# Performance work log

Measured on AMD Instinct MI355X. Metric: run time of the kernel, lower is better.

The kernel has to match this reference:

```python
import jax, jax.numpy as jnp
import numpy as np

PI = float(np.pi)


def _cgs(node_feats, node_centre, nbr_idx, graph_w,
         mean_rho, mean_theta, prec_rho, prec_theta, conv_w, use_graph_weights):
    # node_feats: [B,N,C]; node_centre: [B,N,2]; nbr_idx: [B,N,K] (within-sample node ids)
    # graph_w: [B*N*K, 1] or None; mean/prec: [1,R]; conv_w: [R, C, OUT//R]
    B, N, C = node_feats.shape
    K = nbr_idx.shape[-1]
    R = mean_rho.shape[-1]
    BN = B * N
    # flat neighbor index into B*N nodes (coords[1])
    flat_nbr = (jnp.arange(B, dtype=nbr_idx.dtype)[:, None, None] * N + nbr_idx).reshape(BN * K)
    src = jnp.repeat(jnp.arange(BN), K)
    centre = node_centre.reshape(BN, 2)
    d = centre[src] - centre[flat_nbr]                    # [E,2], node_intersect 'minus'
    rho = jnp.sqrt(d[:, 0] ** 2 + d[:, 1] ** 2)
    theta = jnp.arctan2(d[:, 0], d[:, 1])
    # gaussian mixture edge weights over R kernels
    w_rho = jnp.exp(-0.5 * (rho[:, None] - mean_rho) ** 2 / (1e-14 + prec_rho ** 2))
    first_angle = jnp.abs(theta[:, None] - mean_theta)
    second_angle = jnp.abs(2.0 * PI - first_angle)
    w_theta = jnp.exp(-0.5 * jnp.minimum(first_angle, second_angle) ** 2
                      / (1e-14 + prec_theta ** 2))
    w = w_rho * w_theta
    w = jnp.where(jnp.isnan(w), 0.0, w)
    w = w / jnp.sum(w, axis=1, keepdims=True)             # [E,R]
    if use_graph_weights:
        w = graph_w * w
    ew = w.reshape(BN, K, R)
    nj = node_feats.reshape(BN, C)[flat_nbr].reshape(BN, K, C)   # gather neighbors
    agg = jnp.einsum('ekr,ekc->erc', ew, nj).reshape(B, N, R, C)  # weighted bmm
    out = jnp.einsum('bnrc,rcd->bnrd', agg, conv_w).reshape(B, N, R * conv_w.shape[-1])
    return jax.nn.relu(out)


def setup_inputs() -> dict:
    key = jax.random.key(0)
    ks = jax.random.split(key, 16)
    B, N, K, C, R, OUT = 64, 100, 16, 1024, 8, 1024
    D = OUT // R
    return {
        "node_feats": jax.random.normal(ks[0], (B, N, C), jnp.float32),
        "node_centre": jax.random.uniform(ks[1], (B, N, 2), dtype=jnp.float32),
        "graph_w": jax.random.uniform(ks[2], (B * N * K, 1), dtype=jnp.float32),
        "nbr_idx": jax.random.randint(ks[3], (B, N, K), 0, N, dtype=jnp.int32),
        "mean_rho1": jax.random.uniform(ks[4], (1, R), dtype=jnp.float32),
        "mean_theta1": jax.random.uniform(ks[5], (1, R), dtype=jnp.float32, minval=-PI, maxval=PI),
        "prec_rho1": jax.random.uniform(ks[6], (1, R), dtype=jnp.float32),
        "prec_theta1": jax.random.uniform(ks[7], (1, R), dtype=jnp.float32),
        "conv_w1": jax.random.normal(ks[8], (R, C, D), jnp.float32) * 0.02,
        "mean_rho2": jax.random.uniform(ks[9], (1, R), dtype=jnp.float32),
        "mean_theta2": jax.random.uniform(ks[10], (1, R), dtype=jnp.float32, minval=-PI, maxval=PI),
        "prec_rho2": jax.random.uniform(ks[11], (1, R), dtype=jnp.float32),
        "prec_theta2": jax.random.uniform(ks[12], (1, R), dtype=jnp.float32),
        "conv_w2": jax.random.normal(ks[13], (R, OUT, D), jnp.float32) * 0.02,
    }


def reference(node_feats, node_centre, graph_w,
              mean_rho1, mean_theta1, prec_rho1, prec_theta1, conv_w1,
              mean_rho2, mean_theta2, prec_rho2, prec_theta2, conv_w2,
              nbr_idx):
    # NodeFeatLayer('cgs_sum^8') = Sequential(CgsNodeFeat(use_graph_weights=True),
    #                                          CgsNodeFeat(use_graph_weights=False))
    h = _cgs(node_feats, node_centre, nbr_idx, graph_w,
             mean_rho1, mean_theta1, prec_rho1, prec_theta1, conv_w1, True)
    h = _cgs(h, node_centre, nbr_idx, None,
             mean_rho2, mean_theta2, prec_rho2, prec_theta2, conv_w2, False)
    return h
```

## Files before the change

kernel.cpp:

```cpp
#include <hip/hip_runtime.h>
#include <hip/hip_bf16.h>
#include <math.h>

#define B_   64
#define N_   100
#define K_   16
#define C_   1024
#define R_   8
#define BN_  6400
#define E_   102400

typedef __attribute__((ext_vector_type(8))) short bf16x8;
typedef __attribute__((ext_vector_type(4))) float f32x4;

__device__ __forceinline__ float bf2f(ushort h) {
    union { uint32_t u; float f; } v; v.u = ((uint32_t)h) << 16; return v.f;
}
__device__ __forceinline__ ushort f2bf(float f) {
    union { float f; uint32_t u; } v; v.f = f;
    uint32_t r = v.u + 0x7FFFu + ((v.u >> 16) & 1u);
    return (ushort)(r >> 16);
}

__device__ __forceinline__ void gload_lds16(const void* g, void* l) {
    __builtin_amdgcn_global_load_lds(
        (const __attribute__((address_space(1))) void*)g,
        (__attribute__((address_space(3))) void*)l, 16, 0, 0);
}

__global__ __launch_bounds__(256) void edge_weights_kernel(
        const float* __restrict__ centre, const int* __restrict__ nbr_idx,
        const float* __restrict__ graph_w,
        const float* __restrict__ mr1, const float* __restrict__ mt1,
        const float* __restrict__ pr1, const float* __restrict__ pt1,
        const float* __restrict__ mr2, const float* __restrict__ mt2,
        const float* __restrict__ pr2, const float* __restrict__ pt2,
        float* __restrict__ w1, float* __restrict__ w2) {
    int e = blockIdx.x * blockDim.x + threadIdx.x;
    if (e >= E_) return;
    int n = e / K_;
    int b = n / N_;
    int fn = b * N_ + nbr_idx[e];
    float dx = centre[2*n]   - centre[2*fn];
    float dy = centre[2*n+1] - centre[2*fn+1];
    float rho   = sqrtf(dx*dx + dy*dy);
    float theta = atan2f(dx, dy);
    const float TWO_PI = 6.28318530717958647692f;
    {
        float w[R_]; float s = 0.f;
        #pragma unroll
        for (int r = 0; r < R_; ++r) {
            float dr = rho - mr1[r];
            float wr = expf(-0.5f * dr * dr / (1e-14f + pr1[r]*pr1[r]));
            float fa = fabsf(theta - mt1[r]);
            float mi = fminf(fa, fabsf(TWO_PI - fa));
            float wt = expf(-0.5f * mi * mi / (1e-14f + pt1[r]*pt1[r]));
            float ww = wr * wt;
            if (isnan(ww)) ww = 0.f;
            w[r] = ww; s += ww;
        }
        float gw = graph_w[e];
        #pragma unroll
        for (int r = 0; r < R_; ++r) w1[(size_t)r * E_ + e] = gw * (w[r] / s);
    }
    {
        float w[R_]; float s = 0.f;
        #pragma unroll
        for (int r = 0; r < R_; ++r) {
            float dr = rho - mr2[r];
            float wr = expf(-0.5f * dr * dr / (1e-14f + pr2[r]*pr2[r]));
            float fa = fabsf(theta - mt2[r]);
            float mi = fminf(fa, fabsf(TWO_PI - fa));
            float wt = expf(-0.5f * mi * mi / (1e-14f + pt2[r]*pt2[r]));
            float ww = wr * wt;
            if (isnan(ww)) ww = 0.f;
            w[r] = ww; s += ww;
        }
        #pragma unroll
        for (int r = 0; r < R_; ++r) w2[(size_t)r * E_ + e] = w[r] / s;
    }
}

__global__ __launch_bounds__(256) void cast_x_kernel(
        const float* __restrict__ X, ushort* __restrict__ Xb) {
    int i = (blockIdx.x * 256 + threadIdx.x) * 4;
    float4 v = *(const float4*)&X[i];
    ushort4 o; o.x = f2bf(v.x); o.y = f2bf(v.y); o.z = f2bf(v.z); o.w = f2bf(v.w);
    *(ushort4*)&Xb[i] = o;
}

__global__ __launch_bounds__(256) void wtrans_kernel(
        const float* __restrict__ W1, ushort* __restrict__ Wt1,
        const float* __restrict__ W2, ushort* __restrict__ Wt2) {
    __shared__ ushort T[64][138];
    const float* W = (blockIdx.z == 0) ? W1 : W2;
    ushort*    Wt = (blockIdx.z == 0) ? Wt1 : Wt2;
    int r  = blockIdx.y;
    int c0 = blockIdx.x * 64;
    int t  = threadIdx.x;
    int lane6 = t & 63;
    #pragma unroll
    for (int it = 0; it < 16; ++it) {
        int ch = (t >> 6) + 4 * it;
        int d  = lane6 * 2;
        float2 v = *(const float2*)&W[(((size_t)r << 10) + c0 + ch) * 128 + d];
        T[ch][d]     = f2bf(v.x);
        T[ch][d + 1] = f2bf(v.y);
    }
    __syncthreads();
    #pragma unroll
    for (int it = 0; it < 32; ++it) {
        int d = (t >> 6) + 4 * it;
        Wt[(size_t)(r * 128 + d) * 1024 + c0 + lane6] = T[lane6][d];
    }
}

__global__ __launch_bounds__(256) void fused_gemm_agg_kernel(
        const ushort* __restrict__ Xb,
        const ushort* __restrict__ Wt,
        const float* __restrict__ wR,
        const int*   __restrict__ nbr,
        ushort* __restrict__ outB,
        float*  __restrict__ outF) {
    __shared__ ushort Asb[2][112][32];
    __shared__ ushort Bsb[2][128][32];
    __shared__ ushort P_lds[100][128];
    __shared__ float  w_lds[1600];
    __shared__ int    f_lds[1600];

    int bid = blockIdx.x;
    int swz = (bid & 7) * 64 + (bid >> 3);
    int sample = swz >> 3, cb = swz & 7;
    int t = threadIdx.x, wid = t >> 6, lane = t & 63;

    int srow  = lane >> 2;
    int sslot = (lane & 3) ^ ((lane >> 2) & 3) ^ (lane >> 4);
    int pslot = (lane >> 4) ^ (lane & 3) ^ ((lane >> 2) & 3);

    const ushort* agp = Xb + (size_t)(sample * 100 + srow) * 1024 + sslot * 8;
    const ushort* bgp = Wt + (size_t)(cb * 128 + srow) * 1024 + sslot * 8;

    f32x4 acc[7][2];
    #pragma unroll
    for (int i = 0; i < 7; ++i) { acc[i][0] = (f32x4)0.f; acc[i][1] = (f32x4)0.f; }

    #pragma unroll
    for (int q = 0; q < 2; ++q) {
        int ch = wid + 4 * q;
        if (ch < 7) gload_lds16(agp + (size_t)ch * 16 * 1024, &Asb[0][ch * 16][0]);
        gload_lds16(bgp + (size_t)ch * 16 * 1024, &Bsb[0][ch * 16][0]);
    }
    __syncthreads();

    for (int ts = 0; ts < 32; ++ts) {
        int cur = ts & 1;
        if (ts < 31) {
            int c1 = (ts + 1) * 32;
            #pragma unroll
            for (int q = 0; q < 2; ++q) {
                int ch = wid + 4 * q;
                if (ch < 7) gload_lds16(agp + (size_t)ch * 16 * 1024 + c1,
                                        &Asb[cur ^ 1][ch * 16][0]);
                gload_lds16(bgp + (size_t)ch * 16 * 1024 + c1,
                            &Bsb[cur ^ 1][ch * 16][0]);
            }
        }
        bf16x8 af[7], bfr[2];
        #pragma unroll
        for (int mi = 0; mi < 7; ++mi)
            af[mi] = *(const bf16x8*)&Asb[cur][mi * 16 + (lane & 15)][pslot * 8];
        #pragma unroll
        for (int ni = 0; ni < 2; ++ni)
            bfr[ni] = *(const bf16x8*)&Bsb[cur][wid * 32 + ni * 16 + (lane & 15)][pslot * 8];
        #pragma unroll
        for (int mi = 0; mi < 7; ++mi)
            #pragma unroll
            for (int ni = 0; ni < 2; ++ni)
                acc[mi][ni] = __builtin_amdgcn_mfma_f32_16x16x32_bf16(
                    af[mi], bfr[ni], acc[mi][ni], 0, 0, 0);
        __syncthreads();
    }

    #pragma unroll
    for (int mi = 0; mi < 7; ++mi) {
        #pragma unroll
        for (int ni = 0; ni < 2; ++ni) {
            int colb = wid * 32 + ni * 16 + (lane & 15);
            #pragma unroll
            for (int q = 0; q < 4; ++q) {
                int row = mi * 16 + (lane >> 4) * 4 + q;
                if (row < 100) {
                    int phys = colb ^ (((row >> 2) & 3) << 4);
                    P_lds[row][phys] = f2bf(acc[mi][ni][q]);
                }
            }
        }
    }
    {
        const float* wsrc = wR + (size_t)cb * E_ + (size_t)sample * 1600;
        const int*   nsrc = nbr + (size_t)sample * 1600;
        for (int i = t; i < 1600; i += 256) {
            w_lds[i] = wsrc[i];
            f_lds[i] = nsrc[i];
        }
    }
    __syncthreads();

    int p = lane;
    int nb = wid;
    for (int i = 0; i < 25; ++i) {
        int n = nb + 4 * i;
        float a0 = 0.f, a1 = 0.f;
        #pragma unroll
        for (int k = 0; k < 16; ++k) {
            int row  = f_lds[n * 16 + k];
            float wk = w_lds[n * 16 + k];
            ushort2 v = *(const ushort2*)&P_lds[row][(2 * p) ^ (((row >> 2) & 3) << 4)];
            a0 += wk * bf2f(v.x);
            a1 += wk * bf2f(v.y);
        }
        a0 = fmaxf(a0, 0.f);
        a1 = fmaxf(a1, 0.f);
        size_t base = (size_t)(sample * 100 + n) * 1024 + cb * 128 + 2 * p;
        if (outB) {
            ushort2 o; o.x = f2bf(a0); o.y = f2bf(a1);
            *(ushort2*)&outB[base] = o;
        } else {
            float2 o; o.x = a0; o.y = a1;
            *(float2*)&outF[base] = o;
        }
    }
}

extern "C" void kernel_launch(void* const* d_in, const int* in_sizes, int n_in,
                              void* d_out, int out_size, void* d_ws, size_t ws_size,
                              hipStream_t stream) {
    const float* node_feats = (const float*)d_in[0];
    const float* centre     = (const float*)d_in[1];
    const float* graph_w    = (const float*)d_in[2];
    const int*   nbr_idx    = (const int*)  d_in[3];
    const float* mr1 = (const float*)d_in[4];
    const float* mt1 = (const float*)d_in[5];
    const float* pr1 = (const float*)d_in[6];
    const float* pt1 = (const float*)d_in[7];
    const float* cw1 = (const float*)d_in[8];
    const float* mr2 = (const float*)d_in[9];
    const float* mt2 = (const float*)d_in[10];
    const float* pr2 = (const float*)d_in[11];
    const float* pt2 = (const float*)d_in[12];
    const float* cw2 = (const float*)d_in[13];

    char* ws = (char*)d_ws;
    ushort* Xb  = (ushort*)ws;  ws += (size_t)BN_ * 1024 * 2;
    ushort* W1t = (ushort*)ws;  ws += (size_t)1024 * 1024 * 2;
    ushort* W2t = (ushort*)ws;  ws += (size_t)1024 * 1024 * 2;
    ushort* hb  = (ushort*)ws;  ws += (size_t)BN_ * 1024 * 2;
    float*  w1  = (float*)ws;   ws += (size_t)R_ * E_ * 4;
    float*  w2  = (float*)ws;

    float* out = (float*)d_out;

    edge_weights_kernel<<<(E_ + 255) / 256, 256, 0, stream>>>(
        centre, nbr_idx, graph_w, mr1, mt1, pr1, pt1, mr2, mt2, pr2, pt2, w1, w2);
    cast_x_kernel<<<BN_ * 1024 / 4 / 256, 256, 0, stream>>>(node_feats, Xb);
    wtrans_kernel<<<dim3(16, 8, 2), 256, 0, stream>>>(cw1, W1t, cw2, W2t);

    fused_gemm_agg_kernel<<<512, 256, 0, stream>>>(Xb, W1t, w1, nbr_idx, hb, nullptr);
    fused_gemm_agg_kernel<<<512, 256, 0, stream>>>(hb, W2t, w2, nbr_idx, nullptr, out);
}
```

Measured before the change: 197.4 us.

## Merge prep kernels, pad samples to 128 rows, halve GEMM column tile

The three preprocessing kernels become one launch that branches on block index. Node features are stored padded to 128 rows per sample, so the GEMM A tile loads without masking. The fused GEMM+aggregate kernel now computes 64 output columns per block, on a 2x2 wave layout over 128 padded rows. This doubles the grid to 1024 blocks, and the GEMM staging and aggregation buffers share LDS through a union. The intent is fewer launches, better occupancy and less LDS per block. The cost is that each sample's A tile is reloaded by twice as many blocks, and padded rows waste MFMA work.

```diff
diff --git a/kernel.cpp b/kernel.cpp
--- a/kernel.cpp
+++ b/kernel.cpp
@@ -9,6 +9,7 @@
 #define R_   8
 #define BN_  6400
 #define E_   102400
+#define MPAD 128
 
 typedef __attribute__((ext_vector_type(8))) short bf16x8;
 typedef __attribute__((ext_vector_type(4))) float f32x4;
@@ -21,99 +22,111 @@
     uint32_t r = v.u + 0x7FFFu + ((v.u >> 16) & 1u);
     return (ushort)(r >> 16);
 }
-
 __device__ __forceinline__ void gload_lds16(const void* g, void* l) {
     __builtin_amdgcn_global_load_lds(
         (const __attribute__((address_space(1))) void*)g,
         (__attribute__((address_space(3))) void*)l, 16, 0, 0);
 }
 
-__global__ __launch_bounds__(256) void edge_weights_kernel(
+__global__ __launch_bounds__(256) void prep_kernel(
         const float* __restrict__ centre, const int* __restrict__ nbr_idx,
         const float* __restrict__ graph_w,
         const float* __restrict__ mr1, const float* __restrict__ mt1,
         const float* __restrict__ pr1, const float* __restrict__ pt1,
         const float* __restrict__ mr2, const float* __restrict__ mt2,
         const float* __restrict__ pr2, const float* __restrict__ pt2,
-        float* __restrict__ w1, float* __restrict__ w2) {
-    int e = blockIdx.x * blockDim.x + threadIdx.x;
-    if (e >= E_) return;
-    int n = e / K_;
-    int b = n / N_;
-    int fn = b * N_ + nbr_idx[e];
-    float dx = centre[2*n]   - centre[2*fn];
-    float dy = centre[2*n+1] - centre[2*fn+1];
-    float rho   = sqrtf(dx*dx + dy*dy);
-    float theta = atan2f(dx, dy);
-    const float TWO_PI = 6.28318530717958647692f;
-    {
-        float w[R_]; float s = 0.f;
-        #pragma unroll
-        for (int r = 0; r < R_; ++r) {
-            float dr = rho - mr1[r];
-            float wr = expf(-0.5f * dr * dr / (1e-14f + pr1[r]*pr1[r]));
-            float fa = fabsf(theta - mt1[r]);
-            float mi = fminf(fa, fabsf(TWO_PI - fa));
-            float wt = expf(-0.5f * mi * mi / (1e-14f + pt1[r]*pt1[r]));
-            float ww = wr * wt;
-            if (isnan(ww)) ww = 0.f;
-            w[r] = ww; s += ww;
-        }
-        float gw = graph_w[e];
-        #pragma unroll
-        for (int r = 0; r < R_; ++r) w1[(size_t)r * E_ + e] = gw * (w[r] / s);
-    }
-    {
-        float w[R_]; float s = 0.f;
-        #pragma unroll
-        for (int r = 0; r < R_; ++r) {
-            float dr = rho - mr2[r];
-            float wr = expf(-0.5f * dr * dr / (1e-14f + pr2[r]*pr2[r]));
-            float fa = fabsf(theta - mt2[r]);
-            float mi = fminf(fa, fabsf(TWO_PI - fa));
-            float wt = expf(-0.5f * mi * mi / (1e-14f + pt2[r]*pt2[r]));
-            float ww = wr * wt;
-            if (isnan(ww)) ww = 0.f;
-            w[r] = ww; s += ww;
-        }
-        #pragma unroll
-        for (int r = 0; r < R_; ++r) w2[(size_t)r * E_ + e] = w[r] / s;
-    }
-}
-
-__global__ __launch_bounds__(256) void cast_x_kernel(
-        const float* __restrict__ X, ushort* __restrict__ Xb) {
-    int i = (blockIdx.x * 256 + threadIdx.x) * 4;
-    float4 v = *(const float4*)&X[i];
-    ushort4 o; o.x = f2bf(v.x); o.y = f2bf(v.y); o.z = f2bf(v.z); o.w = f2bf(v.w);
-    *(ushort4*)&Xb[i] = o;
-}
-
-__global__ __launch_bounds__(256) void wtrans_kernel(
-        const float* __restrict__ W1, ushort* __restrict__ Wt1,
-        const float* __restrict__ W2, ushort* __restrict__ Wt2) {
+        const float* __restrict__ X,  const float* __restrict__ CW1,
+        const float* __restrict__ CW2,
+        float* __restrict__ w1, float* __restrict__ w2,
+        ushort* __restrict__ Xb, ushort* __restrict__ Wt1,
+        ushort* __restrict__ Wt2) {
     __shared__ ushort T[64][138];
-    const float* W = (blockIdx.z == 0) ? W1 : W2;
-    ushort*    Wt = (blockIdx.z == 0) ? Wt1 : Wt2;
-    int r  = blockIdx.y;
-    int c0 = blockIdx.x * 64;
-    int t  = threadIdx.x;
-    int lane6 = t & 63;
-    #pragma unroll
-    for (int it = 0; it < 16; ++it) {
-        int ch = (t >> 6) + 4 * it;
-        int d  = lane6 * 2;
-        float2 v = *(const float2*)&W[(((size_t)r << 10) + c0 + ch) * 128 + d];
-        T[ch][d]     = f2bf(v.x);
-        T[ch][d + 1] = f2bf(v.y);
-    }
-    __syncthreads();
-    #pragma unroll
-    for (int it = 0; it < 32; ++it) {
-        int d = (t >> 6) + 4 * it;
-        Wt[(size_t)(r * 128 + d) * 1024 + c0 + lane6] = T[lane6][d];
-    }
-}
+    int bid = blockIdx.x, t = threadIdx.x;
+    if (bid < 400) {
+        int e = bid * 256 + t;
+        int n = e / K_;
+        int b = n / N_;
+        int fn = b * N_ + nbr_idx[e];
+        float dx = centre[2*n]   - centre[2*fn];
+        float dy = centre[2*n+1] - centre[2*fn+1];
+        float rho   = sqrtf(dx*dx + dy*dy);
+        float theta = atan2f(dx, dy);
+        const float TWO_PI = 6.28318530717958647692f;
+        {
+            float w[R_]; float s = 0.f;
+            #pragma unroll
+            for (int r = 0; r < R_; ++r) {
+                float dr = rho - mr1[r];
+                float wr = expf(-0.5f * dr * dr / (1e-14f + pr1[r]*pr1[r]));
+                float fa = fabsf(theta - mt1[r]);
+                float mi = fminf(fa, fabsf(TWO_PI - fa));
+                float wt = expf(-0.5f * mi * mi / (1e-14f + pt1[r]*pt1[r]));
+                float ww = wr * wt;
+                if (isnan(ww)) ww = 0.f;
+                w[r] = ww; s += ww;
+            }
+            float gw = graph_w[e];
+            #pragma unroll
+            for (int r = 0; r < R_; ++r) w1[(size_t)r * E_ + e] = gw * (w[r] / s);
+        }
+        {
+            float w[R_]; float s = 0.f;
+            #pragma unroll
+            for (int r = 0; r < R_; ++r) {
+                float dr = rho - mr2[r];
+                float wr = expf(-0.5f * dr * dr / (1e-14f + pr2[r]*pr2[r]));
+                float fa = fabsf(theta - mt2[r]);
+                float mi = fminf(fa, fabsf(TWO_PI - fa));
+                float wt = expf(-0.5f * mi * mi / (1e-14f + pt2[r]*pt2[r]));
+                float ww = wr * wt;
+                if (isnan(ww)) ww = 0.f;
+                w[r] = ww; s += ww;
+            }
+            #pragma unroll
+            for (int r = 0; r < R_; ++r) w2[(size_t)r * E_ + e] = w[r] / s;
+        }
+    } else if (bid < 3600) {
+        int gid = (bid - 400) * 256 + t;
+        int n  = gid >> 7;
+        int c0 = (gid & 127) * 8;
+        const float* src = X + (size_t)n * 1024 + c0;
+        float4 v0 = *(const float4*)src;
+        float4 v1 = *(const float4*)(src + 4);
+        bf16x8 o;
+        o[0] = (short)f2bf(v0.x); o[1] = (short)f2bf(v0.y);
+        o[2] = (short)f2bf(v0.z); o[3] = (short)f2bf(v0.w);
+        o[4] = (short)f2bf(v1.x); o[5] = (short)f2bf(v1.y);
+        o[6] = (short)f2bf(v1.z); o[7] = (short)f2bf(v1.w);
+        int prow = (n / 100) * MPAD + (n % 100);
+        *(bf16x8*)&Xb[(size_t)prow * 1024 + c0] = o;
+    } else {
+        int w = bid - 3600;
+        int layer = w >> 7, rr = (w >> 4) & 7, ct = w & 15;
+        const float* W = layer ? CW2 : CW1;
+        ushort*    Wt = layer ? Wt2 : Wt1;
+        int c0 = ct * 64;
+        int lane6 = t & 63;
+        #pragma unroll
+        for (int it = 0; it < 16; ++it) {
+            int ch = (t >> 6) + 4 * it;
+            int d  = lane6 * 2;
+            float2 v = *(const float2*)&W[(((size_t)rr << 10) + c0 + ch) * 128 + d];
+            T[ch][d]     = f2bf(v.x);
+            T[ch][d + 1] = f2bf(v.y);
+        }
+        __syncthreads();
+        #pragma unroll
+        for (int it = 0; it < 32; ++it) {
+            int d = (t >> 6) + 4 * it;
+            Wt[(size_t)(rr * 128 + d) * 1024 + c0 + lane6] = T[lane6][d];
+        }
+    }
+}
+
+union SharedU {
+    struct { ushort A[2][128][32]; ushort Bm[2][64][32]; } m;
+    struct { ushort P[100][64]; float w[1600]; int f[1600]; } e;
+};
 
 __global__ __launch_bounds__(256) void fused_gemm_agg_kernel(
         const ushort* __restrict__ Xb,
@@ -122,58 +135,46 @@
         const int*   __restrict__ nbr,
         ushort* __restrict__ outB,
         float*  __restrict__ outF) {
-    __shared__ ushort Asb[2][112][32];
-    __shared__ ushort Bsb[2][128][32];
-    __shared__ ushort P_lds[100][128];
-    __shared__ float  w_lds[1600];
-    __shared__ int    f_lds[1600];
-
+    __shared__ SharedU su;
     int bid = blockIdx.x;
-    int swz = (bid & 7) * 64 + (bid >> 3);
-    int sample = swz >> 3, cb = swz & 7;
+    int swz = (bid & 7) * 128 + (bid >> 3);
+    int sample = swz >> 4, cb = swz & 15;
     int t = threadIdx.x, wid = t >> 6, lane = t & 63;
+    int wm = wid >> 1, wn = wid & 1;
 
     int srow  = lane >> 2;
     int sslot = (lane & 3) ^ ((lane >> 2) & 3) ^ (lane >> 4);
     int pslot = (lane >> 4) ^ (lane & 3) ^ ((lane >> 2) & 3);
 
-    const ushort* agp = Xb + (size_t)(sample * 100 + srow) * 1024 + sslot * 8;
-    const ushort* bgp = Wt + (size_t)(cb * 128 + srow) * 1024 + sslot * 8;
-
-    f32x4 acc[7][2];
+    const ushort* agp = Xb + (size_t)(sample * MPAD + srow) * 1024 + sslot * 8;
+    const ushort* bgp = Wt + (size_t)(cb * 64 + srow) * 1024 + sslot * 8;
+
+    f32x4 acc[4][2];
     #pragma unroll
-    for (int i = 0; i < 7; ++i) { acc[i][0] = (f32x4)0.f; acc[i][1] = (f32x4)0.f; }
-
-    #pragma unroll
-    for (int q = 0; q < 2; ++q) {
-        int ch = wid + 4 * q;
-        if (ch < 7) gload_lds16(agp + (size_t)ch * 16 * 1024, &Asb[0][ch * 16][0]);
-        gload_lds16(bgp + (size_t)ch * 16 * 1024, &Bsb[0][ch * 16][0]);
-    }
+    for (int i = 0; i < 4; ++i) { acc[i][0] = (f32x4)0.f; acc[i][1] = (f32x4)0.f; }
+
+    gload_lds16(agp + (size_t)(wid * 16) * 1024,       &su.m.A[0][wid * 16][0]);
+    gload_lds16(agp + (size_t)((wid + 4) * 16) * 1024, &su.m.A[0][(wid + 4) * 16][0]);
+    gload_lds16(bgp + (size_t)(wid * 16) * 1024,       &su.m.Bm[0][wid * 16][0]);
     __syncthreads();
 
     for (int ts = 0; ts < 32; ++ts) {
         int cur = ts & 1;
         if (ts < 31) {
             int c1 = (ts + 1) * 32;
-            #pragma unroll
-            for (int q = 0; q < 2; ++q) {
-                int ch = wid + 4 * q;
-                if (ch < 7) gload_lds16(agp + (size_t)ch * 16 * 1024 + c1,
-                                        &Asb[cur ^ 1][ch * 16][0]);
-                gload_lds16(bgp + (size_t)ch * 16 * 1024 + c1,
-                            &Bsb[cur ^ 1][ch * 16][0]);
-            }
-        }
-        bf16x8 af[7], bfr[2];
-        #pragma unroll
-        for (int mi = 0; mi < 7; ++mi)
-            af[mi] = *(const bf16x8*)&Asb[cur][mi * 16 + (lane & 15)][pslot * 8];
+            gload_lds16(agp + (size_t)(wid * 16) * 1024 + c1,       &su.m.A[cur ^ 1][wid * 16][0]);
+            gload_lds16(agp + (size_t)((wid + 4) * 16) * 1024 + c1, &su.m.A[cur ^ 1][(wid + 4) * 16][0]);
+            gload_lds16(bgp + (size_t)(wid * 16) * 1024 + c1,       &su.m.Bm[cur ^ 1][wid * 16][0]);
+        }
+        bf16x8 af[4], bfr[2];
+        #pragma unroll
+        for (int mi = 0; mi < 4; ++mi)
+            af[mi] = *(const bf16x8*)&su.m.A[cur][wm * 64 + mi * 16 + (lane & 15)][pslot * 8];
         #pragma unroll
         for (int ni = 0; ni < 2; ++ni)
-            bfr[ni] = *(const bf16x8*)&Bsb[cur][wid * 32 + ni * 16 + (lane & 15)][pslot * 8];
-        #pragma unroll
-        for (int mi = 0; mi < 7; ++mi)
+            bfr[ni] = *(const bf16x8*)&su.m.Bm[cur][wn * 32 + ni * 16 + (lane & 15)][pslot * 8];
+        #pragma unroll
+        for (int mi = 0; mi < 4; ++mi)
             #pragma unroll
             for (int ni = 0; ni < 2; ++ni)
                 acc[mi][ni] = __builtin_amdgcn_mfma_f32_16x16x32_bf16(
@@ -182,52 +183,51 @@
     }
 
     #pragma unroll
-    for (int mi = 0; mi < 7; ++mi) {
+    for (int mi = 0; mi < 4; ++mi) {
         #pragma unroll
         for (int ni = 0; ni < 2; ++ni) {
-            int colb = wid * 32 + ni * 16 + (lane & 15);
+            int col = wn * 32 + ni * 16 + (lane & 15);
             #pragma unroll
             for (int q = 0; q < 4; ++q) {
-                int row = mi * 16 + (lane >> 4) * 4 + q;
-                if (row < 100) {
-                    int phys = colb ^ (((row >> 2) & 3) << 4);
-                    P_lds[row][phys] = f2bf(acc[mi][ni][q]);
-                }
+                int row = wm * 64 + mi * 16 + (lane >> 4) * 4 + q;
+                if (row < 100)
+                    su.e.P[row][col ^ (((row >> 2) & 3) << 4)] = f2bf(acc[mi][ni][q]);
             }
         }
     }
     {
-        const float* wsrc = wR + (size_t)cb * E_ + (size_t)sample * 1600;
+        const float* wsrc = wR + (size_t)(cb >> 1) * E_ + (size_t)sample * 1600;
         const int*   nsrc = nbr + (size_t)sample * 1600;
-        for (int i = t; i < 1600; i += 256) {
-            w_lds[i] = wsrc[i];
-            f_lds[i] = nsrc[i];
+        #pragma unroll
+        for (int q = 0; q < 7; ++q) {
+            int i = t + q * 256;
+            if (i < 1600) { su.e.w[i] = wsrc[i]; su.e.f[i] = nsrc[i]; }
         }
     }
     __syncthreads();
 
-    int p = lane;
-    int nb = wid;
-    for (int i = 0; i < 25; ++i) {
-        int n = nb + 4 * i;
+    int cp = t & 31, ng = t >> 5;
+    int j0 = cp * 2;
+    for (int i = 0; i < 13; ++i) {
+        int n = ng + 8 * i;
+        if (n >= 100) break;
         float a0 = 0.f, a1 = 0.f;
         #pragma unroll
         for (int k = 0; k < 16; ++k) {
-            int row  = f_lds[n * 16 + k];
-            float wk = w_lds[n * 16 + k];
-            ushort2 v = *(const ushort2*)&P_lds[row][(2 * p) ^ (((row >> 2) & 3) << 4)];
+            int row  = su.e.f[n * 16 + k];
+            float wk = su.e.w[n * 16 + k];
+            ushort2 v = *(const ushort2*)&su.e.P[row][j0 ^ (((row >> 2) & 3) << 4)];
             a0 += wk * bf2f(v.x);
             a1 += wk * bf2f(v.y);
         }
         a0 = fmaxf(a0, 0.f);
         a1 = fmaxf(a1, 0.f);
-        size_t base = (size_t)(sample * 100 + n) * 1024 + cb * 128 + 2 * p;
         if (outB) {
             ushort2 o; o.x = f2bf(a0); o.y = f2bf(a1);
-            *(ushort2*)&outB[base] = o;
+            *(ushort2*)&outB[(size_t)(sample * MPAD + n) * 1024 + cb * 64 + j0] = o;
         } else {
             float2 o; o.x = a0; o.y = a1;
-            *(float2*)&outF[base] = o;
+            *(float2*)&outF[(size_t)(sample * 100 + n) * 1024 + cb * 64 + j0] = o;
         }
     }
 }
@@ -251,20 +251,19 @@
     const float* cw2 = (const float*)d_in[13];
 
     char* ws = (char*)d_ws;
-    ushort* Xb  = (ushort*)ws;  ws += (size_t)BN_ * 1024 * 2;
+    ushort* Xb  = (ushort*)ws;  ws += (size_t)B_ * MPAD * 1024 * 2;
+    ushort* hb  = (ushort*)ws;  ws += (size_t)B_ * MPAD * 1024 * 2;
     ushort* W1t = (ushort*)ws;  ws += (size_t)1024 * 1024 * 2;
     ushort* W2t = (ushort*)ws;  ws += (size_t)1024 * 1024 * 2;
-    ushort* hb  = (ushort*)ws;  ws += (size_t)BN_ * 1024 * 2;
     float*  w1  = (float*)ws;   ws += (size_t)R_ * E_ * 4;
     float*  w2  = (float*)ws;
 
     float* out = (float*)d_out;
 
-    edge_weights_kernel<<<(E_ + 255) / 256, 256, 0, stream>>>(
-        centre, nbr_idx, graph_w, mr1, mt1, pr1, pt1, mr2, mt2, pr2, pt2, w1, w2);
-    cast_x_kernel<<<BN_ * 1024 / 4 / 256, 256, 0, stream>>>(node_feats, Xb);
-    wtrans_kernel<<<dim3(16, 8, 2), 256, 0, stream>>>(cw1, W1t, cw2, W2t);
-
-    fused_gemm_agg_kernel<<<512, 256, 0, stream>>>(Xb, W1t, w1, nbr_idx, hb, nullptr);
-    fused_gemm_agg_kernel<<<512, 256, 0, stream>>>(hb, W2t, w2, nbr_idx, nullptr, out);
-}
+    prep_kernel<<<3856, 256, 0, stream>>>(
+        centre, nbr_idx, graph_w, mr1, mt1, pr1, pt1, mr2, mt2, pr2, pt2,
+        node_feats, cw1, cw2, w1, w2, Xb, W1t, W2t);
+
+    fused_gemm_agg_kernel<<<1024, 256, 0, stream>>>(Xb, W1t, w1, nbr_idx, hb, nullptr);
+    fused_gemm_agg_kernel<<<1024, 256, 0, stream>>>(hb, W2t, w2, nbr_idx, nullptr, out);
+}
```

After: 233.6 us. +18.3%, slower.
